# Kernel tuning notes

Measured on AMD Instinct MI355X. Metric: run time of the kernel, lower is better.

Reference implementation:

```python
import jax, jax.numpy as jnp
import numpy as np

D_MODEL, D_STATE, D_CONV, EXPAND = 1024, 16, 4, 2
D_INNER = EXPAND * D_MODEL            # 2048
DT_RANK = D_MODEL // 16               # 64
B, L = 2, 4096


def setup_inputs() -> dict:
    key = jax.random.key(0)
    ks = jax.random.split(key, 8)
    s = 0.02
    u = jax.random.normal(ks[0], (B, L, D_MODEL), jnp.float32)
    in_proj_w = jax.random.normal(ks[1], (2 * D_INNER, D_MODEL), jnp.float32) * s
    conv_w = jax.random.normal(ks[2], (D_INNER, D_CONV), jnp.float32) * 0.2
    conv_b = jnp.zeros((D_INNER,), jnp.float32)
    x_proj_w = jax.random.normal(ks[3], (DT_RANK + 2 * D_STATE, D_INNER), jnp.float32) * s
    dt_proj_w = jax.random.normal(ks[4], (D_INNER, DT_RANK), jnp.float32) * (DT_RANK ** -0.5)
    # dt bias initialized so softplus(dt_bias) in [1e-3, 1e-1], as in mamba-ssm
    dt = jnp.exp(jax.random.uniform(ks[5], (D_INNER,)) * (np.log(0.1) - np.log(1e-3)) + np.log(1e-3))
    dt_bias = jnp.log(-jnp.expm1(-dt) * jnp.exp(dt))  # inverse softplus
    A_log = jnp.log(jnp.tile(jnp.arange(1, D_STATE + 1, dtype=jnp.float32), (D_INNER, 1)))
    D_in = jnp.ones((D_INNER,), jnp.float32)
    out_proj_w = jax.random.normal(ks[6], (D_MODEL, D_INNER), jnp.float32) * s
    D_skip = jnp.ones((D_MODEL,), jnp.float32)
    return dict(u=u, in_proj_w=in_proj_w, conv_w=conv_w, conv_b=conv_b,
                x_proj_w=x_proj_w, dt_proj_w=dt_proj_w, dt_bias=dt_bias,
                A_log=A_log, D_in=D_in, out_proj_w=out_proj_w, D_skip=D_skip)


def _mamba(u, in_proj_w, conv_w, conv_b, x_proj_w, dt_proj_w, dt_bias,
           A_log, D_in, out_proj_w):
    b, l, _ = u.shape
    xz = jnp.einsum('bld,ed->ble', u, in_proj_w)      # (B,L,2*Din)
    x, z = jnp.split(xz, 2, axis=-1)
    # causal depthwise conv1d over time, kernel size D_CONV
    xp = jnp.pad(x, ((0, 0), (D_CONV - 1, 0), (0, 0)))
    x = sum(xp[:, k:k + l, :] * conv_w[:, k] for k in range(D_CONV)) + conv_b
    x = jax.nn.silu(x)
    x_dbl = jnp.einsum('bld,ed->ble', x, x_proj_w)    # (B,L,dt_rank+2N)
    dt = jax.nn.softplus(x_dbl[..., :DT_RANK] @ dt_proj_w.T + dt_bias)  # (B,L,Din)
    Bm = x_dbl[..., DT_RANK:DT_RANK + D_STATE]        # (B,L,N)
    Cm = x_dbl[..., DT_RANK + D_STATE:]               # (B,L,N)
    A = -jnp.exp(A_log)                               # (Din,N)

    def step(h, inp):
        dt_t, B_t, C_t, x_t = inp                     # (B,Din),(B,N),(B,N),(B,Din)
        dA = jnp.exp(dt_t[..., None] * A)             # (B,Din,N)
        h = dA * h + (dt_t * x_t)[..., None] * B_t[:, None, :]
        y = jnp.einsum('bdn,bn->bd', h, C_t)
        return h, y

    h0 = jnp.zeros((b, D_INNER, D_STATE), u.dtype)
    xs = (dt.transpose(1, 0, 2), Bm.transpose(1, 0, 2),
          Cm.transpose(1, 0, 2), x.transpose(1, 0, 2))
    _, ys = jax.lax.scan(step, h0, xs)                # (L,B,Din)
    y = ys.transpose(1, 0, 2) + x * D_in
    y = y * jax.nn.silu(z)
    return jnp.einsum('bld,ed->ble', y, out_proj_w)   # (B,L,D_MODEL)


def reference(u, in_proj_w, conv_w, conv_b, x_proj_w, dt_proj_w, dt_bias,
              A_log, D_in, out_proj_w, D_skip):
    y = _mamba(u, in_proj_w, conv_w, conv_b, x_proj_w, dt_proj_w, dt_bias,
               A_log, D_in, out_proj_w)
    return y + D_skip[None, None, :] * u
```

## Files before the change

kernel.cpp:

```cpp
#include <hip/hip_runtime.h>

typedef unsigned short u16;
typedef unsigned int u32;
typedef __attribute__((ext_vector_type(8))) short s16x8;
typedef __attribute__((ext_vector_type(4))) float f32x4;

__device__ inline u16 f2bf(float f){
    u32 u = __float_as_uint(f);
    u32 r = (u + 0x7fffu + ((u >> 16) & 1u)) >> 16;
    return (u16)r;
}
__device__ inline float bf2f(u16 h){
    return __uint_as_float(((u32)h) << 16);
}

#define GLOAD_LDS16(g, l) __builtin_amdgcn_global_load_lds( \
    (__attribute__((address_space(1))) void*)(void*)(g),    \
    (__attribute__((address_space(3))) void*)(l), 16, 0, 0)

#define MEMFENCE asm volatile("" ::: "memory")

template<int EPI>
__global__ __launch_bounds__(512, 2) void gemm256(
    const u16* __restrict__ A, const u16* __restrict__ B,
    int M, int N, int K, int nbn,
    float* __restrict__ Cf, u16* __restrict__ Cb, u16* __restrict__ Cb2,
    const float* __restrict__ aux0, const float* __restrict__ aux1)
{
    __shared__ u16 lds[2][2][256 * 64];
    const int tid  = threadIdx.x;
    const int lane = tid & 63, wave = tid >> 6;
    const int wr = wave >> 2, wc = wave & 3;
    const int l16 = lane & 15, lg = lane >> 4;

    int wgid = blockIdx.x, nwg = gridDim.x;
    int swz = wgid;
    if ((nwg & 7) == 0) { int cpx = nwg >> 3; swz = (wgid & 7) * cpx + (wgid >> 3); }
    const int bm = swz / nbn, bn = swz % nbn;

    const u16* Ab = A + (size_t)bm * 256 * K;
    const u16* Bb = B + (size_t)bn * 256 * K;

    const int srow   = wave * 8 + (lane >> 3);
    const int scol16 = (lane & 7) ^ ((lane >> 3) & 7);

    auto stageA = [&](int buf, int kt) {
        #pragma unroll
        for (int j = 0; j < 4; j++)
            GLOAD_LDS16(Ab + (size_t)(j * 64 + srow) * K + kt + scol16 * 8,
                        &lds[buf][0][(j * 64 + wave * 8) * 64]);
    };
    auto stageB = [&](int buf, int kt) {
        #pragma unroll
        for (int j = 0; j < 4; j++)
            GLOAD_LDS16(Bb + (size_t)(j * 64 + srow) * K + kt + scol16 * 8,
                        &lds[buf][1][(j * 64 + wave * 8) * 64]);
    };

    f32x4 acc[2][2][4][2] = {};
    s16x8 a[4][2], b0[2][2], b1[2][2];

    auto readA = [&](int buf, int mh) {
        #pragma unroll
        for (int m = 0; m < 4; m++)
            #pragma unroll
            for (int ks = 0; ks < 2; ks++) {
                int row = wr * 128 + mh * 64 + m * 16 + l16;
                int c16 = (ks * 4 + lg) ^ (l16 & 7);
                a[m][ks] = *(const s16x8*)&lds[buf][0][row * 64 + c16 * 8];
            }
    };
    auto readB = [&](int buf, int nh, s16x8 (&b)[2][2]) {
        #pragma unroll
        for (int n = 0; n < 2; n++)
            #pragma unroll
            for (int ks = 0; ks < 2; ks++) {
                int row = wc * 64 + nh * 32 + n * 16 + l16;
                int c16 = (ks * 4 + lg) ^ (l16 & 7);
                b[n][ks] = *(const s16x8*)&lds[buf][1][row * 64 + c16 * 8];
            }
    };

    const int NT = K >> 6;

    stageA(0, 0); stageB(0, 0);
    asm volatile("s_waitcnt vmcnt(0)" ::: "memory");
    __builtin_amdgcn_s_barrier();
    MEMFENCE;

    for (int t = 0; t < NT; t++) {
        const int bufc = t & 1;
        const bool pre = (t < NT - 1);
        #pragma unroll
        for (int p = 0; p < 4; p++) {
            const int mh = (p >> 1) & 1;
            const int nh = (p == 0 || p == 3) ? 0 : 1;
            if (p == 0 && pre) stageA(bufc ^ 1, (t + 1) << 6);
            if (p == 1 && pre) stageB(bufc ^ 1, (t + 1) << 6);
            if (p == 0) { readA(bufc, 0); readB(bufc, 0, b0); }
            if (p == 1) { readB(bufc, 1, b1); }
            if (p == 2) { readA(bufc, 1); }
            if (p == 3 && pre)
                asm volatile("s_waitcnt vmcnt(0)" ::: "memory");
            MEMFENCE;
            __builtin_amdgcn_s_barrier();
            MEMFENCE;
            __builtin_amdgcn_s_setprio(1);
            {
                s16x8 (&bb)[2][2] = (nh == 0) ? b0 : b1;
                #pragma unroll
                for (int m = 0; m < 4; m++)
                    #pragma unroll
                    for (int n = 0; n < 2; n++)
                        #pragma unroll
                        for (int ks = 0; ks < 2; ks++)
                            acc[mh][nh][m][n] = __builtin_amdgcn_mfma_f32_16x16x32_bf16(
                                a[m][ks], bb[n][ks], acc[mh][nh][m][n], 0, 0, 0);
            }
            __builtin_amdgcn_s_setprio(0);
            if (p == 3) {
                MEMFENCE;
                __builtin_amdgcn_s_barrier();
                MEMFENCE;
            }
        }
    }

    #pragma unroll
    for (int mh = 0; mh < 2; mh++)
        #pragma unroll
        for (int nh = 0; nh < 2; nh++)
            #pragma unroll
            for (int m = 0; m < 4; m++)
                #pragma unroll
                for (int n = 0; n < 2; n++) {
                    const int col = bn * 256 + wc * 64 + nh * 32 + n * 16 + l16;
                    #pragma unroll
                    for (int r = 0; r < 4; r++) {
                        const int row = bm * 256 + wr * 128 + mh * 64 + m * 16 + lg * 4 + r;
                        float v = acc[mh][nh][m][n][r];
                        if (EPI == 0) {
                            if (col < 2048) Cb[(size_t)row * 2048 + col] = f2bf(v);
                            else            Cb2[(size_t)row * 2048 + (col - 2048)] = f2bf(v);
                        } else {
                            float o = v + aux0[col] * aux1[(size_t)row * N + col];
                            Cf[(size_t)row * N + col] = o;
                        }
                    }
                }
}

__global__ __launch_bounds__(256) void gemm_dt(
    const u16* __restrict__ A, const u16* __restrict__ B,
    int M, int N, int K,
    u16* __restrict__ Cb, const float* __restrict__ aux0)
{
    constexpr int BK = 64;
    __shared__ u16 As[128 * BK];
    __shared__ u16 Bs[128 * BK];
    const int tid  = threadIdx.x;
    const int lane = tid & 63, wave = tid >> 6;
    const int wr = wave >> 1, wc = wave & 1;
    const int bm = blockIdx.x, bn = blockIdx.y;
    const int l16 = lane & 15, lg = lane >> 4;

    const u16* Ab = A + (size_t)bm * 128 * K;
    const u16* Bb = B + (size_t)bn * 128 * K;

    f32x4 acc[4][4] = {};

    for (int kt = 0; kt < K; kt += BK) {
        #pragma unroll
        for (int p = 0; p < 4; p++) {
            int flat = (p * 256 + tid) * 8;
            int r = flat >> 6, c = flat & 63;
            GLOAD_LDS16(Ab + (size_t)r * K + kt + c, As + flat);
        }
        #pragma unroll
        for (int p = 0; p < 4; p++) {
            int flat = (p * 256 + tid) * 8;
            int r = flat >> 6, c = flat & 63;
            GLOAD_LDS16(Bb + (size_t)r * K + kt + c, Bs + flat);
        }
        asm volatile("s_waitcnt vmcnt(0)" ::: "memory");
        __syncthreads();
        #pragma unroll
        for (int kk = 0; kk < 2; kk++) {
            s16x8 a[4], b[4];
            #pragma unroll
            for (int m = 0; m < 4; m++)
                a[m] = *(const s16x8*)&As[(wr * 64 + m * 16 + l16) * BK + kk * 32 + lg * 8];
            #pragma unroll
            for (int n = 0; n < 4; n++)
                b[n] = *(const s16x8*)&Bs[(wc * 64 + n * 16 + l16) * BK + kk * 32 + lg * 8];
            #pragma unroll
            for (int m = 0; m < 4; m++)
                #pragma unroll
                for (int n = 0; n < 4; n++)
                    acc[m][n] = __builtin_amdgcn_mfma_f32_16x16x32_bf16(a[m], b[n], acc[m][n], 0, 0, 0);
        }
        __syncthreads();
    }

    const int row0 = bm * 128 + wr * 64 + lg * 4;
    const int col0 = bn * 128 + wc * 64 + l16;
    #pragma unroll
    for (int m = 0; m < 4; m++)
        #pragma unroll
        for (int n = 0; n < 4; n++) {
            const int col = col0 + n * 16;
            #pragma unroll
            for (int r = 0; r < 4; r++) {
                const int row = row0 + m * 16 + r;
                float t2 = acc[m][n][r] + aux0[col];
                float sp = (t2 > 15.f) ? t2 : __logf(1.f + __expf(t2));
                Cb[(size_t)row * N + col] = f2bf(sp);
            }
        }
}

__global__ __launch_bounds__(256) void gemm_xproj_sk(
    const u16* __restrict__ A, const u16* __restrict__ B,
    float* __restrict__ part)
{
    constexpr int BK = 64, K = 2048;
    __shared__ u16 As[128 * BK];
    __shared__ u16 Bs[128 * BK];
    const int tid  = threadIdx.x;
    const int lane = tid & 63, wave = tid >> 6;
    const int wr = wave >> 1, wc = wave & 1;
    const int bm = blockIdx.x, sk = blockIdx.y;
    const int l16 = lane & 15, lg = lane >> 4;

    const u16* Ab = A + (size_t)bm * 128 * K;
    const u16* Bb = B;
    const int kt0 = sk * 256;

    f32x4 acc[4][4] = {};

    for (int kt = kt0; kt < kt0 + 256; kt += BK) {
        #pragma unroll
        for (int p = 0; p < 4; p++) {
            int flat = (p * 256 + tid) * 8;
            int r = flat >> 6, c = flat & 63;
            GLOAD_LDS16(Ab + (size_t)r * K + kt + c, As + flat);
        }
        #pragma unroll
        for (int p = 0; p < 4; p++) {
            int flat = (p * 256 + tid) * 8;
            int r = flat >> 6, c = flat & 63;
            GLOAD_LDS16(Bb + (size_t)r * K + kt + c, Bs + flat);
        }
        asm volatile("s_waitcnt vmcnt(0)" ::: "memory");
        __syncthreads();
        #pragma unroll
        for (int kk = 0; kk < 2; kk++) {
            s16x8 a[4], b[4];
            #pragma unroll
            for (int m = 0; m < 4; m++)
                a[m] = *(const s16x8*)&As[(wr * 64 + m * 16 + l16) * BK + kk * 32 + lg * 8];
            #pragma unroll
            for (int n = 0; n < 4; n++)
                b[n] = *(const s16x8*)&Bs[(wc * 64 + n * 16 + l16) * BK + kk * 32 + lg * 8];
            #pragma unroll
            for (int m = 0; m < 4; m++)
                #pragma unroll
                for (int n = 0; n < 4; n++)
                    acc[m][n] = __builtin_amdgcn_mfma_f32_16x16x32_bf16(a[m], b[n], acc[m][n], 0, 0, 0);
        }
        __syncthreads();
    }

    float* pb = part + (size_t)sk * 8192 * 128;
    const int row0 = bm * 128 + wr * 64 + lg * 4;
    const int col0 = wc * 64 + l16;
    #pragma unroll
    for (int m = 0; m < 4; m++)
        #pragma unroll
        for (int n = 0; n < 4; n++)
            #pragma unroll
            for (int r = 0; r < 4; r++)
                pb[(size_t)(row0 + m * 16 + r) * 128 + col0 + n * 16] = acc[m][n][r];
}

__global__ __launch_bounds__(256) void combine_xproj(
    const float* __restrict__ part, u16* __restrict__ dtin,
    float* __restrict__ xBC)
{
    const int gid = blockIdx.x * 256 + threadIdx.x;
    const int row = gid >> 7, col = gid & 127;
    float s = 0.f;
    #pragma unroll
    for (int sk = 0; sk < 8; sk++) s += part[(size_t)sk * 8192 * 128 + gid];
    if (col < 64)      dtin[(size_t)row * 64 + col] = f2bf(s);
    else if (col < 96) xBC[(size_t)row * 32 + (col - 64)] = s;
}

__global__ __launch_bounds__(256) void cvt_all(
    const float* __restrict__ u, const float* __restrict__ Wi,
    const float* __restrict__ Wo, const float* __restrict__ Wdt,
    const float* __restrict__ Wx,
    u16* __restrict__ u_bf, u16* __restrict__ Wi_bf, u16* __restrict__ Wo_bf,
    u16* __restrict__ Wdt_bf, u16* __restrict__ Wx_bf)
{
    size_t i = ((size_t)blockIdx.x * 256 + threadIdx.x) * 4;
    const size_t E0 = 8388608, E1 = E0 + 4194304, E2 = E1 + 2097152, E3 = E2 + 131072;
    f32x4 v;
    u16* dst;
    size_t off;
    if (i < E0)      { off = i;      v = *(const f32x4*)(u + off);   dst = u_bf + off; }
    else if (i < E1) { off = i - E0; v = *(const f32x4*)(Wi + off);  dst = Wi_bf + off; }
    else if (i < E2) { off = i - E1; v = *(const f32x4*)(Wo + off);  dst = Wo_bf + off; }
    else if (i < E3) { off = i - E2; v = *(const f32x4*)(Wdt + off); dst = Wdt_bf + off; }
    else {
        off = i - E3;
        size_t row = off >> 11;
        if (row < 96) v = *(const f32x4*)(Wx + off);
        else          v = (f32x4){0.f, 0.f, 0.f, 0.f};
        dst = Wx_bf + off;
    }
    ushort4 o;
    o.x = f2bf(v[0]); o.y = f2bf(v[1]); o.z = f2bf(v[2]); o.w = f2bf(v[3]);
    *(ushort4*)dst = o;
}

__global__ __launch_bounds__(256) void conv_silu(
    const u16* __restrict__ xzx, const float* __restrict__ cw,
    const float* __restrict__ cb, u16* __restrict__ xc)
{
    const int tid = threadIdx.x;
    const int d0 = tid * 8;
    const int t0 = blockIdx.x * 16;
    const int b  = blockIdx.y;
    float W0[8], W1[8], W2[8], W3[8], BI[8];
    #pragma unroll
    for (int j = 0; j < 8; j++) {
        f32x4 w = *(const f32x4*)(cw + (size_t)(d0 + j) * 4);
        W0[j] = w[0]; W1[j] = w[1]; W2[j] = w[2]; W3[j] = w[3];
        BI[j] = cb[d0 + j];
    }
    const u16* xp = xzx + (size_t)(b * 4096) * 2048 + d0;
    u16* op = xc + (size_t)(b * 4096) * 2048 + d0;

    float x0[8], x1[8], x2[8];
    #pragma unroll
    for (int j = 0; j < 8; j++) { x0[j] = 0.f; x1[j] = 0.f; x2[j] = 0.f; }
    if (t0 >= 3) {
        s16x8 v0 = *(const s16x8*)(xp + (size_t)(t0 - 3) * 2048);
        s16x8 v1 = *(const s16x8*)(xp + (size_t)(t0 - 2) * 2048);
        s16x8 v2 = *(const s16x8*)(xp + (size_t)(t0 - 1) * 2048);
        #pragma unroll
        for (int j = 0; j < 8; j++) {
            x0[j] = bf2f((u16)v0[j]); x1[j] = bf2f((u16)v1[j]); x2[j] = bf2f((u16)v2[j]);
        }
    }
    #pragma unroll
    for (int k = 0; k < 16; k++) {
        int t = t0 + k;
        s16x8 cv = *(const s16x8*)(xp + (size_t)t * 2048);
        s16x8 o;
        #pragma unroll
        for (int j = 0; j < 8; j++) {
            float c = bf2f((u16)cv[j]);
            float s = BI[j] + W0[j] * x0[j] + W1[j] * x1[j] + W2[j] * x2[j] + W3[j] * c;
            float v = s * __fdividef(1.f, 1.f + __expf(-s));
            o[j] = (short)f2bf(v);
            x0[j] = x1[j]; x1[j] = x2[j]; x2[j] = c;
        }
        *(s16x8*)(op + (size_t)t * 2048) = o;
    }
}

__global__ __launch_bounds__(256) void scan_p1(
    const u16* __restrict__ dtb, const u16* __restrict__ xc,
    const float* __restrict__ xBC, const float* __restrict__ A_log,
    u16* __restrict__ Aagg, u16* __restrict__ Bagg)
{
    __shared__ float Bsh[64][16];
    const int tid = threadIdx.x;
    const int d = blockIdx.x * 256 + tid;
    const int c = blockIdx.y, b = blockIdx.z;

    {
        int ti = tid >> 2, p = tid & 3;
        f32x4 bv = *(const f32x4*)(xBC + ((size_t)(b * 4096 + c * 64 + ti)) * 32 + p * 4);
        *(f32x4*)&Bsh[ti][p * 4] = bv;
    }
    __syncthreads();

    float Adn[16];
    #pragma unroll
    for (int q = 0; q < 4; q++) {
        f32x4 al = *(const f32x4*)(A_log + (size_t)d * 16 + q * 4);
        #pragma unroll
        for (int j = 0; j < 4; j++) Adn[q * 4 + j] = -__expf(al[j]);
    }

    const size_t base = (size_t)(b * 4096 + c * 64) * 2048 + d;
    const u16* dtp = dtb + base;
    const u16* xp  = xc  + base;

    float h[16];
    #pragma unroll
    for (int n = 0; n < 16; n++) h[n] = 0.f;
    float sumdt = 0.f;

    float dtv = bf2f(dtp[0]), xv = bf2f(xp[0]);
    for (int t = 0; t < 64; t++) {
        float ndt = 0.f, nx = 0.f;
        if (t < 63) { ndt = bf2f(dtp[(size_t)(t + 1) * 2048]); nx = bf2f(xp[(size_t)(t + 1) * 2048]); }
        float dtx = dtv * xv;
        sumdt += dtv;
        f32x4 B0 = *(const f32x4*)&Bsh[t][0];
        f32x4 B1 = *(const f32x4*)&Bsh[t][4];
        f32x4 B2 = *(const f32x4*)&Bsh[t][8];
        f32x4 B3 = *(const f32x4*)&Bsh[t][12];
        #pragma unroll
        for (int n = 0; n < 16; n++) {
            float Bv = (n < 4) ? B0[n] : (n < 8) ? B1[n - 4] : (n < 12) ? B2[n - 8] : B3[n - 12];
            float aa = __expf(Adn[n] * dtv);
            h[n] = fmaf(aa, h[n], dtx * Bv);
        }
        dtv = ndt; xv = nx;
    }

    const size_t abase = ((size_t)(b * 2048 + d) * 16) * 64 + c;
    #pragma unroll
    for (int n = 0; n < 16; n++) {
        Aagg[abase + (size_t)n * 64] = f2bf(__expf(Adn[n] * sumdt));
        Bagg[abase + (size_t)n * 64] = f2bf(h[n]);
    }
}

__global__ __launch_bounds__(256) void scan_p2(
    const u16* __restrict__ Aagg, u16* __restrict__ BaggH0)
{
    const int gid = blockIdx.x * 256 + threadIdx.x;
    const size_t base = (size_t)gid * 64;
    s16x8 Ar[8], Br[8];
    #pragma unroll
    for (int i = 0; i < 8; i++) {
        Ar[i] = *(const s16x8*)(Aagg + base + i * 8);
        Br[i] = *(const s16x8*)(BaggH0 + base + i * 8);
    }
    s16x8 Hr[8];
    float h = 0.f;
    #pragma unroll
    for (int i = 0; i < 8; i++) {
        #pragma unroll
        for (int j = 0; j < 8; j++) {
            float ac = bf2f((u16)Ar[i][j]);
            float bc = bf2f((u16)Br[i][j]);
            Hr[i][j] = (short)f2bf(h);
            h = fmaf(ac, h, bc);
        }
    }
    #pragma unroll
    for (int i = 0; i < 8; i++)
        *(s16x8*)(BaggH0 + base + i * 8) = Hr[i];
}

__global__ __launch_bounds__(256) void scan_p3(
    const u16* __restrict__ dtb, const u16* __restrict__ xc,
    const float* __restrict__ xBC, const float* __restrict__ A_log,
    const u16* __restrict__ H0, const u16* __restrict__ xzz,
    const float* __restrict__ D_in, u16* __restrict__ yy)
{
    __shared__ float BCs[64][32];
    const int tid = threadIdx.x;
    const int d = blockIdx.x * 256 + tid;
    const int c = blockIdx.y, b = blockIdx.z;

    {
        int ti = tid >> 2, p = tid & 3;
        const float* src = xBC + ((size_t)(b * 4096 + c * 64 + ti)) * 32 + p * 8;
        f32x4 v0 = *(const f32x4*)src;
        f32x4 v1 = *(const f32x4*)(src + 4);
        *(f32x4*)&BCs[ti][p * 8] = v0;
        *(f32x4*)&BCs[ti][p * 8 + 4] = v1;
    }
    __syncthreads();

    float Adn[16];
    #pragma unroll
    for (int q = 0; q < 4; q++) {
        f32x4 al = *(const f32x4*)(A_log + (size_t)d * 16 + q * 4);
        #pragma unroll
        for (int j = 0; j < 4; j++) Adn[q * 4 + j] = -__expf(al[j]);
    }
    const float Dd = D_in[d];

    float h[16];
    const size_t hbase = ((size_t)(b * 2048 + d) * 16) * 64 + c;
    #pragma unroll
    for (int n = 0; n < 16; n++) h[n] = bf2f(H0[hbase + (size_t)n * 64]);

    const size_t base = (size_t)(b * 4096 + c * 64) * 2048 + d;
    const u16* dtp = dtb + base;
    const u16* xp  = xc  + base;
    const u16* zp  = xzz + base;
    u16* yp = yy + base;

    float dtv = bf2f(dtp[0]), xv = bf2f(xp[0]), zv = bf2f(zp[0]);
    for (int t = 0; t < 64; t++) {
        float ndt = 0.f, nx = 0.f, nz = 0.f;
        if (t < 63) {
            ndt = bf2f(dtp[(size_t)(t + 1) * 2048]);
            nx  = bf2f(xp[(size_t)(t + 1) * 2048]);
            nz  = bf2f(zp[(size_t)(t + 1) * 2048]);
        }
        float dtx = dtv * xv;
        f32x4 B0 = *(const f32x4*)&BCs[t][0];
        f32x4 B1 = *(const f32x4*)&BCs[t][4];
        f32x4 B2 = *(const f32x4*)&BCs[t][8];
        f32x4 B3 = *(const f32x4*)&BCs[t][12];
        f32x4 C0 = *(const f32x4*)&BCs[t][16];
        f32x4 C1 = *(const f32x4*)&BCs[t][20];
        f32x4 C2 = *(const f32x4*)&BCs[t][24];
        f32x4 C3 = *(const f32x4*)&BCs[t][28];
        float y = 0.f;
        #pragma unroll
        for (int n = 0; n < 16; n++) {
            float Bv = (n < 4) ? B0[n] : (n < 8) ? B1[n - 4] : (n < 12) ? B2[n - 8] : B3[n - 12];
            float Cv = (n < 4) ? C0[n] : (n < 8) ? C1[n - 4] : (n < 12) ? C2[n - 8] : C3[n - 12];
            float aa = __expf(Adn[n] * dtv);
            h[n] = fmaf(aa, h[n], dtx * Bv);
            y = fmaf(h[n], Cv, y);
        }
        float sz = zv * __fdividef(1.f, 1.f + __expf(-zv));
        float val = fmaf(xv, Dd, y) * sz;
        yp[(size_t)t * 2048] = f2bf(val);
        dtv = ndt; xv = nx; zv = nz;
    }
}

extern "C" void kernel_launch(void* const* d_in, const int* in_sizes, int n_in,
                              void* d_out, int out_size, void* d_ws, size_t ws_size,
                              hipStream_t stream)
{
    const float* u       = (const float*)d_in[0];
    const float* Wi      = (const float*)d_in[1];
    const float* conv_w  = (const float*)d_in[2];
    const float* conv_b  = (const float*)d_in[3];
    const float* Wx      = (const float*)d_in[4];
    const float* Wdt     = (const float*)d_in[5];
    const float* dt_bias = (const float*)d_in[6];
    const float* A_log   = (const float*)d_in[7];
    const float* D_in_   = (const float*)d_in[8];
    const float* Wo      = (const float*)d_in[9];
    const float* D_skip  = (const float*)d_in[10];
    float* out = (float*)d_out;
    (void)in_sizes; (void)n_in; (void)out_size;

    const size_t MB = 1u << 20;
    char* ws = (char*)d_ws;
    u16*   xzx    = (u16*)(ws + 0);
    float* xpart  = (float*)(ws + 0);
    u16*   Aagg   = (u16*)(ws + 0);
    u16*   BaggH0 = (u16*)(ws + 8 * MB);
    u16*   xzz    = (u16*)(ws + 32 * MB);
    u16*   xc     = (u16*)(ws + 64 * MB);
    u16*   u_bf   = (u16*)(ws + 96 * MB);
    u16*   Wi_bf  = (u16*)(ws + 112 * MB);
    u16*   dtb    = (u16*)(ws + 96 * MB);
    u16*   Wx_bf  = (u16*)(ws + 128 * MB);
    u16*   Wdt_bf = (u16*)(ws + 128 * MB + 512 * 1024);
    u16*   yybuf  = (u16*)(ws + 128 * MB);
    float* xBC    = (float*)(ws + 160 * MB);
    u16*   dtin   = (u16*)(ws + 161 * MB);
    u16*   Wo_bf  = (u16*)(ws + 162 * MB);
    const size_t NEED = 166 * MB;
    if (ws_size < NEED) return;

    cvt_all<<<14720, 256, 0, stream>>>(u, Wi, Wo, Wdt, Wx,
                                       u_bf, Wi_bf, Wo_bf, Wdt_bf, Wx_bf);

    gemm256<0><<<512, 512, 0, stream>>>(u_bf, Wi_bf, 8192, 4096, 1024, 16,
                                        nullptr, xzx, xzz, nullptr, nullptr);
    conv_silu<<<dim3(256, 2), 256, 0, stream>>>(xzx, conv_w, conv_b, xc);

    gemm_xproj_sk<<<dim3(64, 8), 256, 0, stream>>>(xc, Wx_bf, xpart);
    combine_xproj<<<4096, 256, 0, stream>>>(xpart, dtin, xBC);

    gemm_dt<<<dim3(64, 16), 256, 0, stream>>>(dtin, Wdt_bf, 8192, 2048, 64,
                                              dtb, dt_bias);

    scan_p1<<<dim3(8, 64, 2), 256, 0, stream>>>(dtb, xc, xBC, A_log, Aagg, BaggH0);
    scan_p2<<<256, 256, 0, stream>>>(Aagg, BaggH0);
    scan_p3<<<dim3(8, 64, 2), 256, 0, stream>>>(dtb, xc, xBC, A_log, BaggH0, xzz,
                                                D_in_, yybuf);

    gemm256<3><<<128, 512, 0, stream>>>(yybuf, Wo_bf, 8192, 1024, 2048, 4,
                                        out, nullptr, nullptr, D_skip, u);
}
```

Measured before the change: 373.5 us.

## Restructure GEMM main loop into half-tile staged, two-K-step unrolled pipeline

Splits the LDS A/B tiles into 128-row halves and issues global-to-LDS loads per half, interleaved across eight MFMA phases covering two K-steps per loop iteration. Each phase is bracketed by barriers, with partial vmcnt waits so loads for the next K-step overlap compute more finely. Launch bounds drop from two workgroups per CU to one, which gives more registers but lowers occupancy. The loop assumes NT is even and depends on careful waitcnt accounting, which risks hazards if the counts are wrong.

```diff
diff --git a/kernel.cpp b/kernel.cpp
--- a/kernel.cpp
+++ b/kernel.cpp
@@ -21,13 +21,13 @@
 #define MEMFENCE asm volatile("" ::: "memory")
 
 template<int EPI>
-__global__ __launch_bounds__(512, 2) void gemm256(
+__global__ __launch_bounds__(512, 1) void gemm256(
     const u16* __restrict__ A, const u16* __restrict__ B,
     int M, int N, int K, int nbn,
     float* __restrict__ Cf, u16* __restrict__ Cb, u16* __restrict__ Cb2,
     const float* __restrict__ aux0, const float* __restrict__ aux1)
 {
-    __shared__ u16 lds[2][2][256 * 64];
+    __shared__ u16 lds[2][2][2][128 * 64];
     const int tid  = threadIdx.x;
     const int lane = tid & 63, wave = tid >> 6;
     const int wr = wave >> 2, wc = wave & 3;
@@ -41,89 +41,103 @@
     const u16* Ab = A + (size_t)bm * 256 * K;
     const u16* Bb = B + (size_t)bn * 256 * K;
 
-    const int srow   = wave * 8 + (lane >> 3);
-    const int scol16 = (lane & 7) ^ ((lane >> 3) & 7);
-
-    auto stageA = [&](int buf, int kt) {
-        #pragma unroll
-        for (int j = 0; j < 4; j++)
-            GLOAD_LDS16(Ab + (size_t)(j * 64 + srow) * K + kt + scol16 * 8,
-                        &lds[buf][0][(j * 64 + wave * 8) * 64]);
-    };
-    auto stageB = [&](int buf, int kt) {
-        #pragma unroll
-        for (int j = 0; j < 4; j++)
-            GLOAD_LDS16(Bb + (size_t)(j * 64 + srow) * K + kt + scol16 * 8,
-                        &lds[buf][1][(j * 64 + wave * 8) * 64]);
+    auto stage_half = [&](int kbuf, int mat, int half, int kt) {
+        const u16* src = mat ? Bb : Ab;
+        #pragma unroll
+        for (int j = 0; j < 2; j++) {
+            int slot = j * 512 + tid;
+            int r = slot >> 3, cg = slot & 7;
+            GLOAD_LDS16(src + (size_t)(half * 128 + r) * K + kt + ((cg ^ (r & 7)) << 3),
+                        &lds[kbuf][mat][half][(j * 512 + wave * 64) * 8]);
+        }
     };
 
     f32x4 acc[2][2][4][2] = {};
     s16x8 a[4][2], b0[2][2], b1[2][2];
 
-    auto readA = [&](int buf, int mh) {
+    auto readA = [&](int kbuf, int mh) {
         #pragma unroll
         for (int m = 0; m < 4; m++)
             #pragma unroll
             for (int ks = 0; ks < 2; ks++) {
-                int row = wr * 128 + mh * 64 + m * 16 + l16;
-                int c16 = (ks * 4 + lg) ^ (l16 & 7);
-                a[m][ks] = *(const s16x8*)&lds[buf][0][row * 64 + c16 * 8];
+                int r = mh * 64 + m * 16 + l16;
+                int cg = (ks * 4 + lg) ^ (l16 & 7);
+                a[m][ks] = *(const s16x8*)&lds[kbuf][0][wr][r * 64 + cg * 8];
             }
     };
-    auto readB = [&](int buf, int nh, s16x8 (&b)[2][2]) {
+    auto readB = [&](int kbuf, int nh, s16x8 (&bb)[2][2]) {
         #pragma unroll
         for (int n = 0; n < 2; n++)
             #pragma unroll
             for (int ks = 0; ks < 2; ks++) {
                 int row = wc * 64 + nh * 32 + n * 16 + l16;
-                int c16 = (ks * 4 + lg) ^ (l16 & 7);
-                b[n][ks] = *(const s16x8*)&lds[buf][1][row * 64 + c16 * 8];
+                int half = row >> 7, r = row & 127;
+                int cg = (ks * 4 + lg) ^ (l16 & 7);
+                bb[n][ks] = *(const s16x8*)&lds[kbuf][1][half][r * 64 + cg * 8];
             }
     };
 
+    auto phase_mfma = [&](int mh, int nh, s16x8 (&bb)[2][2]) {
+        MEMFENCE;
+        __builtin_amdgcn_s_barrier();
+        asm volatile("s_waitcnt lgkmcnt(0)" ::: "memory");
+        __builtin_amdgcn_sched_barrier(0);
+        __builtin_amdgcn_s_setprio(1);
+        #pragma unroll
+        for (int m = 0; m < 4; m++)
+            #pragma unroll
+            for (int n = 0; n < 2; n++)
+                #pragma unroll
+                for (int ks = 0; ks < 2; ks++)
+                    acc[mh][nh][m][n] = __builtin_amdgcn_mfma_f32_16x16x32_bf16(
+                        a[m][ks], bb[n][ks], acc[mh][nh][m][n], 0, 0, 0);
+        __builtin_amdgcn_s_setprio(0);
+        MEMFENCE;
+        __builtin_amdgcn_s_barrier();
+        MEMFENCE;
+    };
+
     const int NT = K >> 6;
 
-    stageA(0, 0); stageB(0, 0);
-    asm volatile("s_waitcnt vmcnt(0)" ::: "memory");
+    stage_half(0, 1, 0, 0); stage_half(0, 1, 1, 0);
+    stage_half(0, 0, 0, 0); stage_half(0, 0, 1, 0);
+    if (NT > 1) {
+        stage_half(1, 1, 0, 64);
+        stage_half(1, 0, 0, 64); stage_half(1, 0, 1, 64);
+    }
+    asm volatile("s_waitcnt vmcnt(6)" ::: "memory");
+    MEMFENCE;
     __builtin_amdgcn_s_barrier();
     MEMFENCE;
 
-    for (int t = 0; t < NT; t++) {
-        const int bufc = t & 1;
-        const bool pre = (t < NT - 1);
-        #pragma unroll
-        for (int p = 0; p < 4; p++) {
-            const int mh = (p >> 1) & 1;
-            const int nh = (p == 0 || p == 3) ? 0 : 1;
-            if (p == 0 && pre) stageA(bufc ^ 1, (t + 1) << 6);
-            if (p == 1 && pre) stageB(bufc ^ 1, (t + 1) << 6);
-            if (p == 0) { readA(bufc, 0); readB(bufc, 0, b0); }
-            if (p == 1) { readB(bufc, 1, b1); }
-            if (p == 2) { readA(bufc, 1); }
-            if (p == 3 && pre)
-                asm volatile("s_waitcnt vmcnt(0)" ::: "memory");
-            MEMFENCE;
-            __builtin_amdgcn_s_barrier();
-            MEMFENCE;
-            __builtin_amdgcn_s_setprio(1);
-            {
-                s16x8 (&bb)[2][2] = (nh == 0) ? b0 : b1;
-                #pragma unroll
-                for (int m = 0; m < 4; m++)
-                    #pragma unroll
-                    for (int n = 0; n < 2; n++)
-                        #pragma unroll
-                        for (int ks = 0; ks < 2; ks++)
-                            acc[mh][nh][m][n] = __builtin_amdgcn_mfma_f32_16x16x32_bf16(
-                                a[m][ks], bb[n][ks], acc[mh][nh][m][n], 0, 0, 0);
-            }
-            __builtin_amdgcn_s_setprio(0);
-            if (p == 3) {
-                MEMFENCE;
-                __builtin_amdgcn_s_barrier();
-                MEMFENCE;
-            }
-        }
+    for (int it = 0; it < (NT >> 1); it++) {
+        const int t1k = (2 * it + 1) << 6;
+        const int t2k = (2 * it + 2) << 6;
+        const int t3k = (2 * it + 3) << 6;
+        const bool pre = (2 * it + 2) < NT;
+        readA(0, 0); readB(0, 0, b0);
+        stage_half(1, 1, 1, t1k);
+        phase_mfma(0, 0, b0);
+        readB(0, 1, b1);
+        phase_mfma(0, 1, b1);
+        readA(0, 1);
+        if (pre) stage_half(0, 1, 0, t2k);
+        phase_mfma(1, 1, b1);
+        if (pre) stage_half(0, 1, 1, t2k);
+        asm volatile("s_waitcnt vmcnt(4)" ::: "memory");
+        phase_mfma(1, 0, b0);
+        readA(1, 0); readB(1, 0, b0);
+        if (pre) stage_half(0, 0, 0, t2k);
+        phase_mfma(0, 0, b0);
+        readB(1, 1, b1);
+        if (pre) stage_half(0, 0, 1, t2k);
+        phase_mfma(0, 1, b1);
+        readA(1, 1);
+        if (pre) stage_half(1, 1, 0, t3k);
+        phase_mfma(1, 1, b1);
+        if (pre) { stage_half(1, 0, 0, t3k); stage_half(1, 0, 1, t3k); }
+        asm volatile("s_waitcnt vmcnt(6)" ::: "memory");
+        phase_mfma(1, 0, b0);
     }
 
     #pragma unroll
```

New measurement: 383.4 us. 1.03x slower.
